# Kernel tuning notes

Measured on AMD Instinct MI355X. Metric: run time of the kernel, lower is better.

Reference implementation:

```python
import jax, jax.numpy as jnp
import numpy as np

FIELD_DIMS = [100000, 50000, 20000, 10000, 5000, 2000, 1000, 500, 100, 10]
FACTOR_DIM = 8
BATCH = 16384
NUM_FIELDS = len(FIELD_DIMS)
INPUT_DIM = int(sum(FIELD_DIMS))
OFFSETS = np.concatenate([[0], np.cumsum(FIELD_DIMS)[:-1]]).astype(np.int32)


def setup_inputs() -> dict:
    key = jax.random.key(0)
    k_x, k_w, k_e = jax.random.split(key, 3)
    # per-field indices, each column in [0, field_dims[f])
    cols = [jax.random.randint(jax.random.fold_in(k_x, f), (BATCH,), 0, d, dtype=jnp.int32)
            for f, d in enumerate(FIELD_DIMS)]
    x = jnp.stack(cols, axis=1)  # (B, F) int32
    # linear: weight (input_dim,), bias scalar (nn.Linear(input_dim, 1))
    w_linear = jax.random.normal(k_w, (INPUT_DIM,), dtype=jnp.float32) * 0.01
    b_linear = jnp.zeros((), dtype=jnp.float32)
    # one embedding table per field: (F, input_dim, D)
    emb = jax.random.normal(k_e, (NUM_FIELDS, INPUT_DIM, FACTOR_DIM), dtype=jnp.float32) * 0.01
    return {"x": x, "w_linear": w_linear, "b_linear": b_linear, "emb": emb}


def reference(x, w_linear, b_linear, emb):
    # x: (B, F) int32 per-field raw indices
    F = emb.shape[0]
    x_off = x + jnp.asarray(OFFSETS, x.dtype)[None, :]  # (B, F) global indices
    # Linear term: scatter-to-onehot + matmul == gather weights and sum
    # (indices are distinct per sample since fields occupy disjoint ranges)
    y_lin = jnp.take(w_linear, x_off, axis=0).sum(axis=1) + b_linear  # (B,)
    # FFM term: all_emb[f, b, g, d] = emb[f, x_off[b, g], d]
    all_emb = jnp.take(emb, x_off, axis=1)          # (F, B, F, D)
    A = jnp.transpose(all_emb, (0, 2, 1, 3))        # (F, F, B, D): A[f, g] = emb_f(x_g)
    prod = (A * jnp.transpose(A, (1, 0, 2, 3))).sum(-1)  # (F, F, B): <emb_f(x_g), emb_g(x_f)>
    mask = jnp.triu(jnp.ones((F, F), prod.dtype), k=1)   # pairs f < g
    y_ffm = (prod * mask[:, :, None]).sum((0, 1))   # (B,)
    return y_lin + y_ffm
```

## Files before the change

### kernel.cpp

```cpp
#include <hip/hip_runtime.h>

#define NUM_FIELDS 10
#define FACTOR_DIM 8
#define BATCH      16384
#define INPUT_DIM  188610
#define NPAIRS     45
#define SPW        4

__device__ __constant__ int c_off40[SPW * NUM_FIELDS] = {
    0, 100000, 150000, 170000, 180000, 185000, 187000, 188000, 188500, 188600,
    0, 100000, 150000, 170000, 180000, 185000, 187000, 188000, 188500, 188600,
    0, 100000, 150000, 170000, 180000, 185000, 187000, 188000, 188500, 188600,
    0, 100000, 150000, 170000, 180000, 185000, 187000, 188000, 188500, 188600};

__device__ __constant__ int c_pf[NPAIRS] = {
    0,0,0,0,0,0,0,0,0,
    1,1,1,1,1,1,1,1,
    2,2,2,2,2,2,2,
    3,3,3,3,3,3,
    4,4,4,4,4,
    5,5,5,5,
    6,6,6,
    7,7,
    8};
__device__ __constant__ int c_pg[NPAIRS] = {
    1,2,3,4,5,6,7,8,9,
    2,3,4,5,6,7,8,9,
    3,4,5,6,7,8,9,
    4,5,6,7,8,9,
    5,6,7,8,9,
    6,7,8,9,
    7,8,9,
    8,9,
    9};

__global__ __launch_bounds__(256) void ffm_kernel(
    const int* __restrict__ x,
    const float* __restrict__ w,
    const float* __restrict__ blin,
    const float* __restrict__ emb,
    float* __restrict__ out)
{
    const int gtid = blockIdx.x * blockDim.x + threadIdx.x;
    const int wave = gtid >> 6;
    const int lane = threadIdx.x & 63;

    const int b0 = wave * SPW;
    if (b0 >= BATCH) return;

    const float bl = *blin;

    const int p  = (lane < NPAIRS) ? lane : 0;
    const int pf = c_pf[p];
    const int pg = c_pg[p];
    const int jl = (lane >= NPAIRS && lane < NPAIRS + NUM_FIELDS) ? (lane - NPAIRS) : 0;

    int idx = 0;
    if (lane < SPW * NUM_FIELDS)
        idx = x[b0 * NUM_FIELDS + lane] + c_off40[lane];

    float4 va0[SPW], va1[SPW], vb0[SPW], vb1[SPW];
    float  wv[SPW];
    #pragma unroll
    for (int s = 0; s < SPW; ++s) {
        const int ig = __shfl(idx, s * NUM_FIELDS + pg);
        const int If = __shfl(idx, s * NUM_FIELDS + pf);
        const int ij = __shfl(idx, s * NUM_FIELDS + jl);
        if (lane < NPAIRS) {
            const float4* pa = reinterpret_cast<const float4*>(
                emb + ((size_t)pf * INPUT_DIM + ig) * FACTOR_DIM);
            const float4* pb = reinterpret_cast<const float4*>(
                emb + ((size_t)pg * INPUT_DIM + If) * FACTOR_DIM);
            va0[s] = pa[0]; va1[s] = pa[1];
            vb0[s] = pb[0]; vb1[s] = pb[1];
            wv[s] = 0.0f;
        } else if (lane < NPAIRS + NUM_FIELDS) {
            wv[s] = w[ij];
        } else {
            wv[s] = 0.0f;
        }
    }

    float res[SPW];
    #pragma unroll
    for (int s = 0; s < SPW; ++s) {
        float v;
        if (lane < NPAIRS) {
            v = va0[s].x * vb0[s].x + va0[s].y * vb0[s].y
              + va0[s].z * vb0[s].z + va0[s].w * vb0[s].w
              + va1[s].x * vb1[s].x + va1[s].y * vb1[s].y
              + va1[s].z * vb1[s].z + va1[s].w * vb1[s].w;
        } else {
            v = wv[s];
        }
        #pragma unroll
        for (int m = 1; m < 64; m <<= 1)
            v += __shfl_xor(v, m);
        res[s] = v;
    }

    if (lane == 0) {
        float4 o = make_float4(res[0] + bl, res[1] + bl, res[2] + bl, res[3] + bl);
        *reinterpret_cast<float4*>(out + b0) = o;
    }
}

extern "C" void kernel_launch(void* const* d_in, const int* in_sizes, int n_in,
                              void* d_out, int out_size, void* d_ws, size_t ws_size,
                              hipStream_t stream) {
    const int*   x    = (const int*)d_in[0];
    const float* w    = (const float*)d_in[1];
    const float* blin = (const float*)d_in[2];
    const float* emb  = (const float*)d_in[3];
    float*       out  = (float*)d_out;

    dim3 block(256);
    dim3 grid((BATCH / SPW + 3) / 4);
    hipLaunchKernelGGL(ffm_kernel, grid, block, 0, stream, x, w, blin, emb, out);
}
```

Baseline: 103.9 us.

## Split each wave into 16-lane groups, one sample per group

Each wave is now split into four 16-lane groups, one sample per group. Each lane handles up to four of the 55 items (45 pair dot products plus 10 linear weights), and the items come from compact signed-char lookup tables. Before, lanes 55-63 did nothing and each sample needed a full 64-lane, 6-step shuffle reduction. Now every lane holds useful work and each sample needs only a 4-step reduction within its group. In exchange there is more per-lane branching, and writes to out become scalar stores from four lanes instead of one float4 store.

New measurement: 103.3 us. About the same (-0.6%).

```diff
diff --git a/kernel.cpp b/kernel.cpp
--- a/kernel.cpp
+++ b/kernel.cpp
@@ -4,7 +4,7 @@
 #define FACTOR_DIM 8
 #define BATCH      16384
 #define INPUT_DIM  188610
-#define NPAIRS     45
+#define NITEMS     55
 #define SPW        4
 
 __device__ __constant__ int c_off40[SPW * NUM_FIELDS] = {
@@ -13,26 +13,22 @@
     0, 100000, 150000, 170000, 180000, 185000, 187000, 188000, 188500, 188600,
     0, 100000, 150000, 170000, 180000, 185000, 187000, 188000, 188500, 188600};
 
-__device__ __constant__ int c_pf[NPAIRS] = {
-    0,0,0,0,0,0,0,0,0,
-    1,1,1,1,1,1,1,1,
-    2,2,2,2,2,2,2,
-    3,3,3,3,3,3,
-    4,4,4,4,4,
-    5,5,5,5,
-    6,6,6,
-    7,7,
-    8};
-__device__ __constant__ int c_pg[NPAIRS] = {
-    1,2,3,4,5,6,7,8,9,
-    2,3,4,5,6,7,8,9,
-    3,4,5,6,7,8,9,
-    4,5,6,7,8,9,
-    5,6,7,8,9,
-    6,7,8,9,
-    7,8,9,
-    8,9,
-    9};
+__device__ __constant__ signed char c_tA[NITEMS] = {
+    0,0,0,0,0,0,0,0,0, 1,1,1,1,1,1,1,1, 2,2,2,2,2,2,2, 3,3,3,3,3,3,
+    4,4,4,4,4, 5,5,5,5, 6,6,6, 7,7, 8,
+    -1,-1,-1,-1,-1,-1,-1,-1,-1,-1};
+__device__ __constant__ signed char c_sA[NITEMS] = {
+    1,2,3,4,5,6,7,8,9, 2,3,4,5,6,7,8,9, 3,4,5,6,7,8,9, 4,5,6,7,8,9,
+    5,6,7,8,9, 6,7,8,9, 7,8,9, 8,9, 9,
+    0,1,2,3,4,5,6,7,8,9};
+__device__ __constant__ signed char c_tB[NITEMS] = {
+    1,2,3,4,5,6,7,8,9, 2,3,4,5,6,7,8,9, 3,4,5,6,7,8,9, 4,5,6,7,8,9,
+    5,6,7,8,9, 6,7,8,9, 7,8,9, 8,9, 9,
+    0,0,0,0,0,0,0,0,0,0};
+__device__ __constant__ signed char c_sB[NITEMS] = {
+    0,0,0,0,0,0,0,0,0, 1,1,1,1,1,1,1,1, 2,2,2,2,2,2,2, 3,3,3,3,3,3,
+    4,4,4,4,4, 5,5,5,5, 6,6,6, 7,7, 8,
+    0,0,0,0,0,0,0,0,0,0};
 
 __global__ __launch_bounds__(256) void ffm_kernel(
     const int* __restrict__ x,
@@ -41,68 +37,65 @@
     const float* __restrict__ emb,
     float* __restrict__ out)
 {
-    const int gtid = blockIdx.x * blockDim.x + threadIdx.x;
-    const int wave = gtid >> 6;
+    const int wave = (blockIdx.x * blockDim.x + threadIdx.x) >> 6;
     const int lane = threadIdx.x & 63;
+    const int grp  = lane >> 4;
+    const int gl   = lane & 15;
 
     const int b0 = wave * SPW;
     if (b0 >= BATCH) return;
 
     const float bl = *blin;
 
-    const int p  = (lane < NPAIRS) ? lane : 0;
-    const int pf = c_pf[p];
-    const int pg = c_pg[p];
-    const int jl = (lane >= NPAIRS && lane < NPAIRS + NUM_FIELDS) ? (lane - NPAIRS) : 0;
-
     int idx = 0;
     if (lane < SPW * NUM_FIELDS)
         idx = x[b0 * NUM_FIELDS + lane] + c_off40[lane];
 
-    float4 va0[SPW], va1[SPW], vb0[SPW], vb1[SPW];
-    float  wv[SPW];
+    float4 a0[4], a1[4], bv0[4], bv1[4];
+    float  wv[4];
+    bool   ispair[4];
     #pragma unroll
-    for (int s = 0; s < SPW; ++s) {
-        const int ig = __shfl(idx, s * NUM_FIELDS + pg);
-        const int If = __shfl(idx, s * NUM_FIELDS + pf);
-        const int ij = __shfl(idx, s * NUM_FIELDS + jl);
-        if (lane < NPAIRS) {
+    for (int k = 0; k < 4; ++k) {
+        const int it  = gl + 16 * k;
+        const bool act = (it < NITEMS);
+        const int ii  = act ? it : 0;
+        const int tA = c_tA[ii], sA = c_sA[ii];
+        const int tB = c_tB[ii], sB = c_sB[ii];
+        const int ia = __shfl(idx, grp * NUM_FIELDS + sA);
+        const int ib = __shfl(idx, grp * NUM_FIELDS + sB);
+        wv[k] = 0.0f;
+        ispair[k] = act && (tA >= 0);
+        if (ispair[k]) {
             const float4* pa = reinterpret_cast<const float4*>(
-                emb + ((size_t)pf * INPUT_DIM + ig) * FACTOR_DIM);
+                emb + ((size_t)tA * INPUT_DIM + ia) * FACTOR_DIM);
             const float4* pb = reinterpret_cast<const float4*>(
-                emb + ((size_t)pg * INPUT_DIM + If) * FACTOR_DIM);
-            va0[s] = pa[0]; va1[s] = pa[1];
-            vb0[s] = pb[0]; vb1[s] = pb[1];
-            wv[s] = 0.0f;
-        } else if (lane < NPAIRS + NUM_FIELDS) {
-            wv[s] = w[ij];
-        } else {
-            wv[s] = 0.0f;
+                emb + ((size_t)tB * INPUT_DIM + ib) * FACTOR_DIM);
+            a0[k] = pa[0]; a1[k] = pa[1];
+            bv0[k] = pb[0]; bv1[k] = pb[1];
+        } else if (act) {
+            wv[k] = w[ia];
         }
     }
 
-    float res[SPW];
+    float val = 0.0f;
     #pragma unroll
-    for (int s = 0; s < SPW; ++s) {
-        float v;
-        if (lane < NPAIRS) {
-            v = va0[s].x * vb0[s].x + va0[s].y * vb0[s].y
-              + va0[s].z * vb0[s].z + va0[s].w * vb0[s].w
-              + va1[s].x * vb1[s].x + va1[s].y * vb1[s].y
-              + va1[s].z * vb1[s].z + va1[s].w * vb1[s].w;
+    for (int k = 0; k < 4; ++k) {
+        if (ispair[k]) {
+            val += a0[k].x * bv0[k].x + a0[k].y * bv0[k].y
+                 + a0[k].z * bv0[k].z + a0[k].w * bv0[k].w
+                 + a1[k].x * bv1[k].x + a1[k].y * bv1[k].y
+                 + a1[k].z * bv1[k].z + a1[k].w * bv1[k].w;
         } else {
-            v = wv[s];
+            val += wv[k];
         }
-        #pragma unroll
-        for (int m = 1; m < 64; m <<= 1)
-            v += __shfl_xor(v, m);
-        res[s] = v;
     }
 
-    if (lane == 0) {
-        float4 o = make_float4(res[0] + bl, res[1] + bl, res[2] + bl, res[3] + bl);
-        *reinterpret_cast<float4*>(out + b0) = o;
-    }
+    val += __shfl_xor(val, 1);
+    val += __shfl_xor(val, 2);
+    val += __shfl_xor(val, 4);
+    val += __shfl_xor(val, 8);
+
+    if (gl == 0) out[b0 + grp] = val + bl;
 }
 
 extern "C" void kernel_launch(void* const* d_in, const int* in_sizes, int n_in,
@@ -115,6 +108,6 @@
     float*       out  = (float*)d_out;
 
     dim3 block(256);
-    dim3 grid((BATCH / SPW + 3) / 4);
+    dim3 grid(BATCH / SPW / 4);
     hipLaunchKernelGGL(ffm_kernel, grid, block, 0, stream, x, w, blin, emb, out);
 }
```
